# Performance work log

Measured on AMD Instinct MI355X. Metric: run time of the kernel, lower is better.

## Reference

```python
import jax, jax.numpy as jnp
import numpy as np

N_NODES = 100000
N_EDGES = 1600000
D = 128


def sage_conv(x, src, dst, W_l, W_r, b):
    # mean aggregation of source-node features at destination nodes
    msgs = x[src]  # [E, D] gather
    agg = jax.ops.segment_sum(msgs, dst, num_segments=N_NODES)  # [N, D]
    deg = jax.ops.segment_sum(jnp.ones((src.shape[0],), x.dtype), dst,
                              num_segments=N_NODES)
    agg = agg / jnp.maximum(deg, 1.0)[:, None]
    # PyG SAGEConv: lin_l(agg) + lin_r(x) (bias lives in lin_l)
    return agg @ W_l + x @ W_r + b


def setup_inputs() -> dict:
    key = jax.random.key(0)
    ks = jax.random.split(key, 8)
    s = 1.0 / np.sqrt(D)
    x = jax.random.normal(ks[0], (N_NODES, D), dtype=jnp.float32)
    edge_index = jax.random.randint(ks[1], (2, N_EDGES), 0, N_NODES, dtype=jnp.int64)
    W_l1 = jax.random.normal(ks[2], (D, D), dtype=jnp.float32) * s
    W_r1 = jax.random.normal(ks[3], (D, D), dtype=jnp.float32) * s
    b1 = jnp.zeros((D,), dtype=jnp.float32)
    W_l2 = jax.random.normal(ks[4], (D, D), dtype=jnp.float32) * s
    W_r2 = jax.random.normal(ks[5], (D, D), dtype=jnp.float32) * s
    b2 = jnp.zeros((D,), dtype=jnp.float32)
    return {"x": x, "edge_index": edge_index, "W_l1": W_l1, "W_r1": W_r1,
            "b1": b1, "W_l2": W_l2, "W_r2": W_r2, "b2": b2}


def reference(x, edge_index, W_l1, W_r1, b1, W_l2, W_r2, b2):
    src, dst = edge_index[0], edge_index[1]
    h = jax.nn.relu(sage_conv(x, src, dst, W_l1, W_r1, b1))
    h = jax.nn.relu(sage_conv(h, src, dst, W_l2, W_r2, b2))
    return h
```

## Files before the change

### kernel.cpp

```cpp
#include <hip/hip_runtime.h>
#include <hip/hip_bf16.h>
#include <stdint.h>

#define D 128
#define BCAP 18432
typedef unsigned short u16;
typedef unsigned int u32;
typedef __attribute__((ext_vector_type(8))) short bf16x8;
typedef __attribute__((ext_vector_type(4))) float f32x4;

__device__ inline float bf16lo_to_f(u32 v) {
    u32 u = v << 16; return __builtin_bit_cast(float, u);
}
__device__ inline float bf16hi_to_f(u32 v) {
    u32 u = v & 0xFFFF0000u; return __builtin_bit_cast(float, u);
}
__device__ inline u16 f_to_bf16(float f) {
    u32 u = __builtin_bit_cast(u32, f);
    u += 0x7FFFu + ((u >> 16) & 1u);
    return (u16)(u >> 16);
}
__device__ inline u32 pack_bf16(float a, float b) {
    return (u32)f_to_bf16(a) | ((u32)f_to_bf16(b) << 16);
}

__global__ void zero_ints(int* __restrict__ p, int n) {
    int i = blockIdx.x * blockDim.x + threadIdx.x;
    if (i < n) p[i] = 0;
}

__global__ __launch_bounds__(256) void bin_edges(
    const int* __restrict__ src, const int* __restrict__ dst, int E, int nbuck,
    uint2* __restrict__ pairs, int* __restrict__ bcur) {
    __shared__ int hist[128], gb[128], loc[128];
    int tid = threadIdx.x;
    if (tid < 128) { hist[tid] = 0; loc[tid] = 0; }
    __syncthreads();
    int base = blockIdx.x * 4096;
    int d[16], b[16];
    #pragma unroll
    for (int i = 0; i < 16; ++i) {
        int e = base + i * 256 + tid;
        d[i] = (e < E) ? dst[e] : -1;
        b[i] = (d[i] >= 0) ? (d[i] >> 10) : -1;
        if (b[i] >= 0) atomicAdd(&hist[b[i]], 1);
    }
    __syncthreads();
    if (tid < nbuck && hist[tid] > 0) gb[tid] = atomicAdd(&bcur[tid], hist[tid]);
    __syncthreads();
    #pragma unroll
    for (int i = 0; i < 16; ++i) {
        if (b[i] >= 0) {
            int e = base + i * 256 + tid;
            int s = src[e];
            int r = atomicAdd(&loc[b[i]], 1);
            int pos = gb[b[i]] + r;
            if (pos < BCAP)
                pairs[(size_t)b[i] * BCAP + pos] = make_uint2((u32)s, (u32)d[i]);
        }
    }
}

__global__ __launch_bounds__(256) void build_csr(
    const uint2* __restrict__ pairs, const int* __restrict__ bcur, int N,
    int* __restrict__ cnt, int* __restrict__ seg_start, int* __restrict__ gtotal,
    int* __restrict__ csr_src) {
    __shared__ int cnt_l[1024];
    __shared__ int off_l[1024];
    __shared__ int sblk[256];
    __shared__ int gbase_s;
    int tid = threadIdx.x;
    int bk = blockIdx.x;
    int n0 = bk << 10;
    int nN = min(1024, N - n0);
    #pragma unroll
    for (int i = 0; i < 4; ++i) cnt_l[tid * 4 + i] = 0;
    __syncthreads();
    int m = min(bcur[bk], BCAP);
    const uint2* P = pairs + (size_t)bk * BCAP;
    for (int i = tid; i < m; i += 256) {
        uint2 p = P[i];
        atomicAdd(&cnt_l[(int)p.y - n0], 1);
    }
    __syncthreads();
    int c0 = cnt_l[tid * 4], c1 = cnt_l[tid * 4 + 1], c2 = cnt_l[tid * 4 + 2], c3 = cnt_l[tid * 4 + 3];
    int mysum = c0 + c1 + c2 + c3;
    sblk[tid] = mysum;
    for (int off = 1; off < 256; off <<= 1) {
        __syncthreads();
        int u = (tid >= off) ? sblk[tid - off] : 0;
        __syncthreads();
        sblk[tid] += u;
    }
    int excl = sblk[tid] - mysum;
    off_l[tid * 4]     = excl;
    off_l[tid * 4 + 1] = excl + c0;
    off_l[tid * 4 + 2] = excl + c0 + c1;
    off_l[tid * 4 + 3] = excl + c0 + c1 + c2;
    if (tid == 255) gbase_s = atomicAdd(gtotal, sblk[255]);
    __syncthreads();
    int gbase = gbase_s;
    #pragma unroll
    for (int i = 0; i < 4; ++i) {
        int j = tid * 4 + i;
        if (j < nN) {
            cnt[n0 + j] = cnt_l[j];
            seg_start[n0 + j] = gbase + off_l[j];
        }
    }
    __syncthreads();
    #pragma unroll
    for (int i = 0; i < 4; ++i) cnt_l[tid * 4 + i] = 0;
    __syncthreads();
    for (int i = tid; i < m; i += 256) {
        uint2 p = P[i];
        int dl = (int)p.y - n0;
        int r = atomicAdd(&cnt_l[dl], 1);
        csr_src[gbase + off_l[dl] + r] = (int)p.x;
    }
}

__global__ void convert_x(const float* __restrict__ x, u16* __restrict__ xb, int n2) {
    int i = blockIdx.x * blockDim.x + threadIdx.x;
    if (i >= n2) return;
    float2 v = ((const float2*)x)[i];
    ((u32*)xb)[i] = pack_bf16(v.x, v.y);
}

__global__ void convert_w(const float* __restrict__ Wl1, const float* __restrict__ Wr1,
                          const float* __restrict__ Wl2, const float* __restrict__ Wr2,
                          u16* __restrict__ WT1, u16* __restrict__ WT2) {
    int id = blockIdx.x * blockDim.x + threadIdx.x;
    if (id >= 2 * 128 * 256) return;
    int which = id >> 15;
    int rem = id & 32767;
    int n = rem >> 8;
    int k = rem & 255;
    const float* Wl = which ? Wl2 : Wl1;
    const float* Wr = which ? Wr2 : Wr1;
    float v = (k < 128) ? Wl[k * 128 + n] : Wr[(k - 128) * 128 + n];
    u16* WT = which ? WT2 : WT1;
    WT[n * 256 + k] = f_to_bf16(v);
}

__global__ void aggregate_bf16(const u16* __restrict__ xb, const int* __restrict__ csr_src,
                               const int* __restrict__ seg_start, const int* __restrict__ cnt,
                               int N, u16* __restrict__ agg) {
    int wave = threadIdx.x >> 6;
    int lane = threadIdx.x & 63;
    int n = blockIdx.x * (blockDim.x >> 6) + wave;
    if (n >= N) return;
    int s0 = seg_start[n];
    int deg = cnt[n];
    int sub = lane & 15;
    int eoff = lane >> 4;

    float acc[8] = {0.f, 0.f, 0.f, 0.f, 0.f, 0.f, 0.f, 0.f};

    for (int c0 = 0; c0 < deg; c0 += 64) {
        int chunkN = min(deg - c0, 64);
        int myidx = (lane < chunkN) ? csr_src[s0 + c0 + lane] : 0;
        for (int e0 = 0; e0 < chunkN; e0 += 4) {
            int e = e0 + eoff;
            int s = __shfl(myidx, e & 63);
            if (e < chunkN) {
                uint4 v = ((const uint4*)(xb + (size_t)s * 128))[sub];
                acc[0] += bf16lo_to_f(v.x); acc[1] += bf16hi_to_f(v.x);
                acc[2] += bf16lo_to_f(v.y); acc[3] += bf16hi_to_f(v.y);
                acc[4] += bf16lo_to_f(v.z); acc[5] += bf16hi_to_f(v.z);
                acc[6] += bf16lo_to_f(v.w); acc[7] += bf16hi_to_f(v.w);
            }
        }
    }

    #pragma unroll
    for (int i = 0; i < 8; ++i) {
        acc[i] += __shfl_xor(acc[i], 16);
        acc[i] += __shfl_xor(acc[i], 32);
    }

    if (eoff == 0) {
        float inv = 1.0f / fmaxf((float)deg, 1.0f);
        uint4 o;
        o.x = pack_bf16(acc[0] * inv, acc[1] * inv);
        o.y = pack_bf16(acc[2] * inv, acc[3] * inv);
        o.z = pack_bf16(acc[4] * inv, acc[5] * inv);
        o.w = pack_bf16(acc[6] * inv, acc[7] * inv);
        ((uint4*)(agg + (size_t)n * 128))[sub] = o;
    }
}

template<int OUT_BF16>
__global__ __launch_bounds__(256) void sage_gemm(
    const u16* __restrict__ Aa, const u16* __restrict__ Ax,
    const u16* __restrict__ WT, const float* __restrict__ bias,
    void* __restrict__ out, int N) {
    __shared__ u16 Bl[128 * 256];
    int tid = threadIdx.x;

    {
        const uint4* Wg = (const uint4*)WT;
        uint4* Bl4 = (uint4*)Bl;
        #pragma unroll
        for (int i = 0; i < 16; ++i) {
            int cid = tid + 256 * i;
            int n = cid >> 5;
            int kc = cid & 31;
            Bl4[(n << 5) | (kc ^ (n & 15))] = Wg[cid];
        }
    }
    __syncthreads();

    int wavein = tid >> 6;
    int lane = tid & 63;
    int col = lane & 15;
    int chunk = lane >> 4;
    int wid = blockIdx.x * 4 + wavein;

    size_t m0 = (size_t)wid * 32 + col;
    size_t m1 = m0 + 16;
    size_t m0c = (m0 < (size_t)N) ? m0 : (size_t)(N - 1);
    size_t m1c = (m1 < (size_t)N) ? m1 : (size_t)(N - 1);

    const bf16x8* a0p = (const bf16x8*)(Aa + m0c * 128 + chunk * 8);
    const bf16x8* a1p = (const bf16x8*)(Aa + m1c * 128 + chunk * 8);
    const bf16x8* x0p = (const bf16x8*)(Ax + m0c * 128 + chunk * 8);
    const bf16x8* x1p = (const bf16x8*)(Ax + m1c * 128 + chunk * 8);

    f32x4 acc0[8], acc1[8];
    #pragma unroll
    for (int t = 0; t < 8; ++t) {
        acc0[t] = (f32x4){0.f, 0.f, 0.f, 0.f};
        acc1[t] = (f32x4){0.f, 0.f, 0.f, 0.f};
    }

    #pragma unroll
    for (int s = 0; s < 4; ++s) {
        bf16x8 a0 = a0p[s * 4];
        bf16x8 a1 = a1p[s * 4];
        int kc = s * 4 + chunk;
        #pragma unroll
        for (int t = 0; t < 8; ++t) {
            const bf16x8* bp = (const bf16x8*)(Bl + (((16 * t + col) << 8) | ((kc ^ col) << 3)));
            bf16x8 b = *bp;
            acc0[t] = __builtin_amdgcn_mfma_f32_16x16x32_bf16(a0, b, acc0[t], 0, 0, 0);
            acc1[t] = __builtin_amdgcn_mfma_f32_16x16x32_bf16(a1, b, acc1[t], 0, 0, 0);
        }
    }
    #pragma unroll
    for (int s = 0; s < 4; ++s) {
        bf16x8 a0 = x0p[s * 4];
        bf16x8 a1 = x1p[s * 4];
        int kc = 16 + s * 4 + chunk;
        #pragma unroll
        for (int t = 0; t < 8; ++t) {
            const bf16x8* bp = (const bf16x8*)(Bl + (((16 * t + col) << 8) | ((kc ^ col) << 3)));
            bf16x8 b = *bp;
            acc0[t] = __builtin_amdgcn_mfma_f32_16x16x32_bf16(a0, b, acc0[t], 0, 0, 0);
            acc1[t] = __builtin_amdgcn_mfma_f32_16x16x32_bf16(a1, b, acc1[t], 0, 0, 0);
        }
    }

    #pragma unroll
    for (int mt = 0; mt < 2; ++mt) {
        size_t row0 = (size_t)wid * 32 + mt * 16 + chunk * 4;
        #pragma unroll
        for (int t = 0; t < 8; ++t) {
            int n = 16 * t + col;
            float bv = bias[n];
            f32x4 a = mt ? acc1[t] : acc0[t];
            #pragma unroll
            for (int r = 0; r < 4; ++r) {
                size_t row = row0 + r;
                if (row < (size_t)N) {
                    float v = fmaxf(a[r] + bv, 0.f);
                    if (OUT_BF16) ((u16*)out)[row * 128 + n] = f_to_bf16(v);
                    else          ((float*)out)[row * 128 + n] = v;
                }
            }
        }
    }
}

extern "C" void kernel_launch(void* const* d_in, const int* in_sizes, int n_in,
                              void* d_out, int out_size, void* d_ws, size_t ws_size,
                              hipStream_t stream) {
    const float* x   = (const float*)d_in[0];
    const int*   ei  = (const int*)d_in[1];
    const float* Wl1 = (const float*)d_in[2];
    const float* Wr1 = (const float*)d_in[3];
    const float* b1  = (const float*)d_in[4];
    const float* Wl2 = (const float*)d_in[5];
    const float* Wr2 = (const float*)d_in[6];
    const float* b2  = (const float*)d_in[7];
    float* out       = (float*)d_out;

    int N = in_sizes[0] / D;
    int E = in_sizes[1] / 2;
    const int* src = ei;
    const int* dst = ei + E;
    int nbuck = (N + 1023) >> 10;

    char* ws = (char*)d_ws;
    int* cnt       = (int*)ws;  ws += (size_t)N * 4;
    int* seg_start = (int*)ws;  ws += (size_t)N * 4;
    int* bcur      = (int*)ws;  ws += 128 * 4;
    int* gtotal    = (int*)ws;  ws += 4 * 4;
    ws = (char*)(((uintptr_t)ws + 255) & ~(uintptr_t)255);
    int* csr_src   = (int*)ws;  ws += (size_t)E * 4;
    ws = (char*)(((uintptr_t)ws + 255) & ~(uintptr_t)255);
    u16* WT1       = (u16*)ws;  ws += (size_t)128 * 256 * 2;
    u16* WT2       = (u16*)ws;  ws += (size_t)128 * 256 * 2;
    ws = (char*)(((uintptr_t)ws + 255) & ~(uintptr_t)255);
    u16* aggb      = (u16*)ws;  ws += (size_t)N * 128 * 2;
    ws = (char*)(((uintptr_t)ws + 255) & ~(uintptr_t)255);
    u16* h1b       = (u16*)ws;  ws += (size_t)N * 128 * 2;
    u16* xb        = (u16*)d_out;
    uint2* pairs   = (uint2*)aggb;

    zero_ints<<<1, 256, 0, stream>>>(bcur, 132);

    bin_edges<<<(E + 4095) / 4096, 256, 0, stream>>>(src, dst, E, nbuck, pairs, bcur);
    build_csr<<<nbuck, 256, 0, stream>>>(pairs, bcur, N, cnt, seg_start, gtotal, csr_src);

    convert_x<<<(N * 64 + 255) / 256, 256, 0, stream>>>(x, xb, N * 64);
    convert_w<<<(2 * 128 * 256 + 255) / 256, 256, 0, stream>>>(Wl1, Wr1, Wl2, Wr2, WT1, WT2);

    int aggBlocks = (N + 3) / 4;
    int gemmBlocks = (N + 127) / 128;

    aggregate_bf16<<<aggBlocks, 256, 0, stream>>>(xb, csr_src, seg_start, cnt, N, aggb);
    sage_gemm<1><<<gemmBlocks, 256, 0, stream>>>(aggb, xb, WT1, b1, h1b, N);

    aggregate_bf16<<<aggBlocks, 256, 0, stream>>>(h1b, csr_src, seg_start, cnt, N, aggb);
    sage_gemm<0><<<gemmBlocks, 256, 0, stream>>>(aggb, h1b, WT2, b2, out, N);
}
```

Before: 350.6 us.

## Fuse edge binning with x/W conversion and batch gathers in aggregation

Merges the edge-binning, x-to-bf16 and weight-transpose kernels into one launch that dispatches by block index, cutting two launches and letting the independent prep work overlap. The x conversion now uses float4 loads in a grid-stride loop. The aggregation kernel issues four neighbour-row loads before accumulating, which raises memory-level parallelism, and accumulates with packed float2 vector adds. In exchange it uses more registers in aggregation and needs a clamped shuffle index for inactive lanes.

```diff
diff --git a/kernel.cpp b/kernel.cpp
--- a/kernel.cpp
+++ b/kernel.cpp
@@ -8,6 +8,8 @@
 typedef unsigned int u32;
 typedef __attribute__((ext_vector_type(8))) short bf16x8;
 typedef __attribute__((ext_vector_type(4))) float f32x4;
+typedef __attribute__((ext_vector_type(2))) float f32x2;
+typedef __attribute__((ext_vector_type(2))) unsigned int u32x2;
 
 __device__ inline float bf16lo_to_f(u32 v) {
     u32 u = v << 16; return __builtin_bit_cast(float, u);
@@ -29,34 +31,63 @@
     if (i < n) p[i] = 0;
 }
 
-__global__ __launch_bounds__(256) void bin_edges(
-    const int* __restrict__ src, const int* __restrict__ dst, int E, int nbuck,
-    uint2* __restrict__ pairs, int* __restrict__ bcur) {
+__global__ __launch_bounds__(256) void prep_fused(
+    const int* __restrict__ src, const int* __restrict__ dst, int E, int nbuck, int binB,
+    uint2* __restrict__ pairs, int* __restrict__ bcur,
+    const float* __restrict__ x, u16* __restrict__ xb, int nf4, int convB,
+    const float* __restrict__ Wl1, const float* __restrict__ Wr1,
+    const float* __restrict__ Wl2, const float* __restrict__ Wr2,
+    u16* __restrict__ WT1, u16* __restrict__ WT2) {
     __shared__ int hist[128], gb[128], loc[128];
     int tid = threadIdx.x;
-    if (tid < 128) { hist[tid] = 0; loc[tid] = 0; }
-    __syncthreads();
-    int base = blockIdx.x * 4096;
-    int d[16], b[16];
-    #pragma unroll
-    for (int i = 0; i < 16; ++i) {
-        int e = base + i * 256 + tid;
-        d[i] = (e < E) ? dst[e] : -1;
-        b[i] = (d[i] >= 0) ? (d[i] >> 10) : -1;
-        if (b[i] >= 0) atomicAdd(&hist[b[i]], 1);
-    }
-    __syncthreads();
-    if (tid < nbuck && hist[tid] > 0) gb[tid] = atomicAdd(&bcur[tid], hist[tid]);
-    __syncthreads();
-    #pragma unroll
-    for (int i = 0; i < 16; ++i) {
-        if (b[i] >= 0) {
+    int bid = blockIdx.x;
+    if (bid < binB) {
+        if (tid < 128) { hist[tid] = 0; loc[tid] = 0; }
+        __syncthreads();
+        int base = bid * 4096;
+        int d[16], b[16];
+        #pragma unroll
+        for (int i = 0; i < 16; ++i) {
             int e = base + i * 256 + tid;
-            int s = src[e];
-            int r = atomicAdd(&loc[b[i]], 1);
-            int pos = gb[b[i]] + r;
-            if (pos < BCAP)
-                pairs[(size_t)b[i] * BCAP + pos] = make_uint2((u32)s, (u32)d[i]);
+            d[i] = (e < E) ? dst[e] : -1;
+            b[i] = (d[i] >= 0) ? (d[i] >> 10) : -1;
+            if (b[i] >= 0) atomicAdd(&hist[b[i]], 1);
+        }
+        __syncthreads();
+        if (tid < nbuck && hist[tid] > 0) gb[tid] = atomicAdd(&bcur[tid], hist[tid]);
+        __syncthreads();
+        #pragma unroll
+        for (int i = 0; i < 16; ++i) {
+            if (b[i] >= 0) {
+                int e = base + i * 256 + tid;
+                int s = src[e];
+                int r = atomicAdd(&loc[b[i]], 1);
+                int pos = gb[b[i]] + r;
+                if (pos < BCAP)
+                    pairs[(size_t)b[i] * BCAP + pos] = make_uint2((u32)s, (u32)d[i]);
+            }
+        }
+    } else if (bid < binB + convB) {
+        int idx = (bid - binB) * 256 + tid;
+        int stride = convB * 256;
+        const float4* xf = (const float4*)x;
+        uint2* xo = (uint2*)xb;
+        for (int i = idx; i < nf4; i += stride) {
+            float4 v = xf[i];
+            xo[i] = make_uint2(pack_bf16(v.x, v.y), pack_bf16(v.z, v.w));
+        }
+    } else {
+        int id = (bid - binB - convB) * 256 + tid;
+        if (id < 2 * 128 * 256) {
+            int which = id >> 15;
+            int rem = id & 32767;
+            int n = rem >> 8;
+            int k = rem & 255;
+            const float* Wl = which ? Wl2 : Wl1;
+            const float* Wr = which ? Wr2 : Wr1;
+            float v = (k < 128) ? Wl[k * 128 + n] : Wr[(k - 128) * 128 + n];
+            u16* WT = which ? WT2 : WT1;
+            WT[n * 256 + k] = f_to_bf16(v);
         }
     }
 }
@@ -120,32 +151,10 @@
     }
 }
 
-__global__ void convert_x(const float* __restrict__ x, u16* __restrict__ xb, int n2) {
-    int i = blockIdx.x * blockDim.x + threadIdx.x;
-    if (i >= n2) return;
-    float2 v = ((const float2*)x)[i];
-    ((u32*)xb)[i] = pack_bf16(v.x, v.y);
-}
-
-__global__ void convert_w(const float* __restrict__ Wl1, const float* __restrict__ Wr1,
-                          const float* __restrict__ Wl2, const float* __restrict__ Wr2,
-                          u16* __restrict__ WT1, u16* __restrict__ WT2) {
-    int id = blockIdx.x * blockDim.x + threadIdx.x;
-    if (id >= 2 * 128 * 256) return;
-    int which = id >> 15;
-    int rem = id & 32767;
-    int n = rem >> 8;
-    int k = rem & 255;
-    const float* Wl = which ? Wl2 : Wl1;
-    const float* Wr = which ? Wr2 : Wr1;
-    float v = (k < 128) ? Wl[k * 128 + n] : Wr[(k - 128) * 128 + n];
-    u16* WT = which ? WT2 : WT1;
-    WT[n * 256 + k] = f_to_bf16(v);
-}
-
-__global__ void aggregate_bf16(const u16* __restrict__ xb, const int* __restrict__ csr_src,
-                               const int* __restrict__ seg_start, const int* __restrict__ cnt,
-                               int N, u16* __restrict__ agg) {
+__global__ __launch_bounds__(256) void aggregate_bf16(
+    const u16* __restrict__ xb, const int* __restrict__ csr_src,
+    const int* __restrict__ seg_start, const int* __restrict__ cnt,
+    int N, u16* __restrict__ agg) {
     int wave = threadIdx.x >> 6;
     int lane = threadIdx.x & 63;
     int n = blockIdx.x * (blockDim.x >> 6) + wave;
@@ -155,37 +164,55 @@
     int sub = lane & 15;
     int eoff = lane >> 4;
 
-    float acc[8] = {0.f, 0.f, 0.f, 0.f, 0.f, 0.f, 0.f, 0.f};
+    f32x2 acc2[4];
+    #pragma unroll
+    for (int i = 0; i < 4; ++i) acc2[i] = (f32x2){0.f, 0.f};
 
     for (int c0 = 0; c0 < deg; c0 += 64) {
         int chunkN = min(deg - c0, 64);
         int myidx = (lane < chunkN) ? csr_src[s0 + c0 + lane] : 0;
-        for (int e0 = 0; e0 < chunkN; e0 += 4) {
-            int e = e0 + eoff;
-            int s = __shfl(myidx, e & 63);
-            if (e < chunkN) {
-                uint4 v = ((const uint4*)(xb + (size_t)s * 128))[sub];
-                acc[0] += bf16lo_to_f(v.x); acc[1] += bf16hi_to_f(v.x);
-                acc[2] += bf16lo_to_f(v.y); acc[3] += bf16hi_to_f(v.y);
-                acc[4] += bf16lo_to_f(v.z); acc[5] += bf16hi_to_f(v.z);
-                acc[6] += bf16lo_to_f(v.w); acc[7] += bf16hi_to_f(v.w);
+        for (int e0 = 0; e0 < chunkN; e0 += 16) {
+            uint4 v[4];
+            bool act[4];
+            #pragma unroll
+            for (int j = 0; j < 4; ++j) {
+                int ej = e0 + j * 4 + eoff;
+                act[j] = (ej < chunkN);
+                if (e0 + j * 4 < chunkN) {
+                    int es = act[j] ? ej : (chunkN - 1);
+                    int s = __shfl(myidx, es & 63);
+                    v[j] = ((const uint4*)(xb + (size_t)s * 128))[sub];
+                }
             }
-        }
-    }
-
+            #pragma unroll
+            for (int j = 0; j < 4; ++j) {
+                if (act[j]) {
+                    u32 w;
+                    w = v[j].x; acc2[0] += __builtin_bit_cast(f32x2, (u32x2){w << 16, w & 0xFFFF0000u});
+                    w = v[j].y; acc2[1] += __builtin_bit_cast(f32x2, (u32x2){w << 16, w & 0xFFFF0000u});
+                    w = v[j].z; acc2[2] += __builtin_bit_cast(f32x2, (u32x2){w << 16, w & 0xFFFF0000u});
+                    w = v[j].w; acc2[3] += __builtin_bit_cast(f32x2, (u32x2){w << 16, w & 0xFFFF0000u});
+                }
+            }
+        }
+    }
+
+    float a[8];
+    #pragma unroll
+    for (int i = 0; i < 4; ++i) { a[2 * i] = acc2[i].x; a[2 * i + 1] = acc2[i].y; }
     #pragma unroll
     for (int i = 0; i < 8; ++i) {
-        acc[i] += __shfl_xor(acc[i], 16);
-        acc[i] += __shfl_xor(acc[i], 32);
+        a[i] += __shfl_xor(a[i], 16);
+        a[i] += __shfl_xor(a[i], 32);
     }
 
     if (eoff == 0) {
         float inv = 1.0f / fmaxf((float)deg, 1.0f);
         uint4 o;
-        o.x = pack_bf16(acc[0] * inv, acc[1] * inv);
-        o.y = pack_bf16(acc[2] * inv, acc[3] * inv);
-        o.z = pack_bf16(acc[4] * inv, acc[5] * inv);
-        o.w = pack_bf16(acc[6] * inv, acc[7] * inv);
+        o.x = pack_bf16(a[0] * inv, a[1] * inv);
+        o.y = pack_bf16(a[2] * inv, a[3] * inv);
+        o.z = pack_bf16(a[4] * inv, a[5] * inv);
+        o.w = pack_bf16(a[6] * inv, a[7] * inv);
         ((uint4*)(agg + (size_t)n * 128))[sub] = o;
     }
 }
@@ -320,11 +347,14 @@
 
     zero_ints<<<1, 256, 0, stream>>>(bcur, 132);
 
-    bin_edges<<<(E + 4095) / 4096, 256, 0, stream>>>(src, dst, E, nbuck, pairs, bcur);
+    int binB  = (E + 4095) / 4096;
+    int convB = 2048;
+    int nf4   = N * (D / 4);
+    prep_fused<<<binB + convB + 256, 256, 0, stream>>>(
+        src, dst, E, nbuck, binB, pairs, bcur,
+        x, xb, nf4, convB, Wl1, Wr1, Wl2, Wr2, WT1, WT2);
+
     build_csr<<<nbuck, 256, 0, stream>>>(pairs, bcur, N, cnt, seg_start, gtotal, csr_src);
-
-    convert_x<<<(N * 64 + 255) / 256, 256, 0, stream>>>(x, xb, N * 64);
-    convert_w<<<(2 * 128 * 256 + 255) / 256, 256, 0, stream>>>(Wl1, Wr1, Wl2, Wr2, WT1, WT2);
 
     int aggBlocks = (N + 3) / 4;
     int gemmBlocks = (N + 127) / 128;
```

Measured after the change: 344.8 us. Within noise of the previous version (-1.7%).
